# Optimization experiments

Hardware: AMD Instinct MI355X
Metric: run time of the kernel (lower is better)

Reference implementation:

```python
import jax, jax.numpy as jnp
import numpy as np

BN_EPS = 1e-5


def _conv1x1(x, w, b):
    # x: (B, Cin, H, W), w: (Cout, Cin), b: (Cout,)
    return jnp.einsum('bchw,oc->bohw', x, w) + b[None, :, None, None]


def _maxpool2(x):
    b, c, h, w = x.shape
    return x.reshape(b, c, h // 2, 2, w // 2, 2).max(axis=(3, 5))


def setup_inputs() -> dict:
    key = jax.random.key(0)
    ks = jax.random.split(key, 12)
    B, Cc, Cg, H, W = 16, 20, 256, 80, 80
    Ci, Cig = Cc // 2, Cg // 2  # 10, 128
    return {
        'x_c': jax.random.uniform(ks[0], (B, Cc, H, W), jnp.float32),
        'x_1': jax.random.uniform(ks[1], (B, Cg, H, W), jnp.float32),
        'theta_w': jax.random.normal(ks[2], (Ci, Cc), jnp.float32) * 0.1,
        'theta_b': jax.random.normal(ks[3], (Ci,), jnp.float32) * 0.1,
        'phi_w': jax.random.normal(ks[4], (Ci, Cc), jnp.float32) * 0.1,
        'phi_b': jax.random.normal(ks[5], (Ci,), jnp.float32) * 0.1,
        'g_w': jax.random.normal(ks[6], (Cig, Cg), jnp.float32) * 0.05,
        'g_b': jax.random.normal(ks[7], (Cig,), jnp.float32) * 0.05,
        'W_w': jax.random.normal(ks[8], (Cg, Cig), jnp.float32) * 0.05,
        'W_b': jax.random.normal(ks[9], (Cg,), jnp.float32) * 0.05,
        'bn_gamma': jax.random.uniform(ks[10], (Cg,), jnp.float32),
        'bn_beta': jax.random.normal(ks[11], (Cg,), jnp.float32) * 0.1,
    }


def reference(x_c, x_1, theta_w, theta_b, phi_w, phi_b, g_w, g_b, W_w, W_b, bn_gamma, bn_beta):
    B, _, H, W = x_1.shape
    Cig = g_w.shape[0]
    # g path: conv1x1 on x_1 then 2x2 maxpool -> (B, Np, Cig), Np = (H/2)*(W/2)
    g_x = _maxpool2(_conv1x1(x_1, g_w, g_b)).reshape(B, Cig, -1).transpose(0, 2, 1)
    # theta: (B, N, Ci) with N = H*W; phi: (B, Ci, Np)
    theta_x = _conv1x1(x_c, theta_w, theta_b).reshape(B, theta_w.shape[0], -1).transpose(0, 2, 1)
    phi_x = _maxpool2(_conv1x1(x_c, phi_w, phi_b)).reshape(B, phi_w.shape[0], -1)
    f = jnp.einsum('bnc,bcm->bnm', theta_x, phi_x)  # (B, 6400, 1600)
    attn = jax.nn.softmax(f, axis=-1)
    y = jnp.einsum('bnm,bmc->bnc', attn, g_x)  # (B, N, Cig)
    y = y.transpose(0, 2, 1).reshape(B, Cig, H, W)
    # W: conv1x1 + BatchNorm2d (training mode, biased variance)
    w_y = _conv1x1(y, W_w, W_b)
    mean = w_y.mean(axis=(0, 2, 3))
    var = w_y.var(axis=(0, 2, 3))
    w_y = (w_y - mean[None, :, None, None]) * jax.lax.rsqrt(var + BN_EPS)[None, :, None, None]
    w_y = w_y * bn_gamma[None, :, None, None] + bn_beta[None, :, None, None]
    return w_y + x_1
```

## Files before the change

### kernel.cpp

```cpp
#include <hip/hip_runtime.h>
#include <math.h>

#define BB 16
#define CC 20
#define CI 10
#define CG 256
#define CIG 128
#define HH 80
#define WW 80
#define NN 6400
#define HP 40
#define WPD 40
#define NP 1600
#define CNT (BB*NN)

#define OFF_THETA 0
#define OFF_PHI   (OFF_THETA + BB*CI*NN)
#define OFF_Y     (OFF_PHI + BB*CI*NP)
#define OFF_SUMY  (OFF_Y + BB*NN*CIG)
#define OFF_MYY   (OFF_SUMY + 128)
#define OFF_A     (OFF_MYY + 128*128)
#define OFF_BC    (OFF_A + 256)
#define OFF_GW16  (OFF_BC + 256)
#define OFF_WW16  (OFF_GW16 + CG*CIG/2)
#define OFF_GT    (OFF_WW16 + CG*CIG/2)
#define OFF_PARTS (OFF_GT + BB*CIG*NP/2)

typedef _Float16 f16x8 __attribute__((ext_vector_type(8)));
typedef float f32x4 __attribute__((ext_vector_type(4)));
typedef float f32x16 __attribute__((ext_vector_type(16)));

__global__ void k0_prep(const float* __restrict__ gw,
                        const float* __restrict__ ww,
                        float* __restrict__ ws) {
    int idx = blockIdx.x * 256 + threadIdx.x;
    if (idx < CG * CIG) {
        int co = idx / CG, ci = idx % CG;
        _Float16* gw16 = (_Float16*)(ws + OFF_GW16);
        gw16[(ci >> 5) * (CIG * 32) + co * 32 + (ci & 31)] = (_Float16)gw[idx];
        _Float16* ww16 = (_Float16*)(ws + OFF_WW16);
        ww16[idx] = (_Float16)ww[idx];
    }
}

__global__ __launch_bounds__(256) void k1_theta(const float* __restrict__ xc,
                                                const float* __restrict__ tw,
                                                const float* __restrict__ tb,
                                                float* __restrict__ ws) {
    __shared__ float w[CI * CC];
    __shared__ float bia[CI];
    int t = threadIdx.x;
    if (t < CI * CC) w[t] = tw[t];
    if (t < CI) bia[t] = tb[t];
    __syncthreads();
    int idx = blockIdx.x * 256 + t;
    int b = idx / NN, n = idx % NN;
    float acc[CI];
#pragma unroll
    for (int o = 0; o < CI; o++) acc[o] = bia[o];
#pragma unroll
    for (int c = 0; c < CC; c++) {
        float x = xc[(b * CC + c) * NN + n];
#pragma unroll
        for (int o = 0; o < CI; o++) acc[o] += w[o * CC + c] * x;
    }
#pragma unroll
    for (int o = 0; o < CI; o++) ws[OFF_THETA + (b * CI + o) * NN + n] = acc[o];
}

__global__ __launch_bounds__(256) void k1_phi(const float* __restrict__ xc,
                                              const float* __restrict__ pw,
                                              const float* __restrict__ pb,
                                              float* __restrict__ ws) {
    __shared__ float w[CI * CC];
    __shared__ float bia[CI];
    int t = threadIdx.x;
    if (t < CI * CC) w[t] = pw[t];
    if (t < CI) bia[t] = pb[t];
    __syncthreads();
    int idx = blockIdx.x * 256 + t;
    int b = idx / NP, mp = idx % NP;
    int hp = mp / WPD, wp = mp % WPD;
    float best[CI];
#pragma unroll
    for (int o = 0; o < CI; o++) best[o] = -1e30f;
#pragma unroll
    for (int p = 0; p < 4; p++) {
        int n = (2 * hp + (p >> 1)) * WW + 2 * wp + (p & 1);
        float acc[CI];
#pragma unroll
        for (int o = 0; o < CI; o++) acc[o] = bia[o];
#pragma unroll
        for (int c = 0; c < CC; c++) {
            float x = xc[(b * CC + c) * NN + n];
#pragma unroll
            for (int o = 0; o < CI; o++) acc[o] += w[o * CC + c] * x;
        }
#pragma unroll
        for (int o = 0; o < CI; o++) best[o] = fmaxf(best[o], acc[o]);
    }
#pragma unroll
    for (int o = 0; o < CI; o++) ws[OFF_PHI + (b * CI + o) * NP + mp] = best[o];
}

__global__ __launch_bounds__(256) void k2_convg(const float* __restrict__ x1,
                                                const float* __restrict__ gb,
                                                float* __restrict__ ws) {
    __shared__ _Float16 smem[21760];
    const int t = threadIdx.x;
    const int w = t >> 6, l = t & 63, h = l >> 5, ln = l & 31;
    const int bid = blockIdx.x;
    const int b = bid / 40, nb = bid % 40;
    const int n0 = nb * 160;
    const ushort* gw16 = (const ushort*)(ws + OFF_GW16);
    const float* xsrc = x1 + (size_t)b * CG * NN + n0;

    f32x16 acc[5];
#pragma unroll
    for (int j = 0; j < 5; j++)
#pragma unroll
        for (int r = 0; r < 16; r++) acc[j][r] = 0.f;

    const int bk = t >> 3, bs = t & 7;
    uint4 ar[2];
    float4 br[5];

#define K2_LOAD(kc)                                                              \
    {                                                                            \
        ar[0] = *(const uint4*)(gw16 + (kc) * 4096 + t * 16);                    \
        ar[1] = *(const uint4*)(gw16 + (kc) * 4096 + t * 16 + 8);                \
        const float* xr = xsrc + (size_t)((kc) * 32 + bk) * NN + bs * 20;        \
        br[0] = *(const float4*)(xr);                                            \
        br[1] = *(const float4*)(xr + 4);                                        \
        br[2] = *(const float4*)(xr + 8);                                        \
        br[3] = *(const float4*)(xr + 12);                                       \
        br[4] = *(const float4*)(xr + 16);                                       \
    }
#define K2_WRITE(p)                                                              \
    {                                                                            \
        _Float16* Ap = smem + (p) * 10368;                                       \
        _Float16* Bp = Ap + 4608;                                                \
        _Float16* ad = Ap + (t >> 1) * 36 + (t & 1) * 16;                        \
        *(uint2*)(ad + 0) = make_uint2(ar[0].x, ar[0].y);                        \
        *(uint2*)(ad + 4) = make_uint2(ar[0].z, ar[0].w);                        \
        *(uint2*)(ad + 8) = make_uint2(ar[1].x, ar[1].y);                        \
        *(uint2*)(ad + 12) = make_uint2(ar[1].z, ar[1].w);                       \
        _Float16* bd = Bp + bk;                                                  \
        for (int i = 0; i < 5; i++) {                                            \
            int nbase = bs * 20 + 4 * i;                                         \
            bd[(nbase + 0) * 36] = (_Float16)br[i].x;                            \
            bd[(nbase + 1) * 36] = (_Float16)br[i].y;                            \
            bd[(nbase + 2) * 36] = (_Float16)br[i].z;                            \
            bd[(nbase + 3) * 36] = (_Float16)br[i].w;                            \
        }                                                                        \
    }

    K2_LOAD(0);
    K2_WRITE(0);
    __syncthreads();

    for (int kc = 0; kc < 8; ++kc) {
        if (kc < 7) K2_LOAD(kc + 1);
        {
            const _Float16* Ap = smem + (kc & 1) * 10368;
            const _Float16* Bp = Ap + 4608;
#pragma unroll
            for (int kk = 0; kk < 2; kk++) {
                union { f16x8 v; uint2 q[2]; } a;
                const _Float16* ap = Ap + (w * 32 + ln) * 36 + kk * 16 + 8 * h;
                a.q[0] = *(const uint2*)(ap);
                a.q[1] = *(const uint2*)(ap + 4);
#pragma unroll
                for (int j = 0; j < 5; j++) {
                    union { f16x8 v; uint2 q[2]; } bb;
                    const _Float16* bp = Bp + (j * 32 + ln) * 36 + kk * 16 + 8 * h;
                    bb.q[0] = *(const uint2*)(bp);
                    bb.q[1] = *(const uint2*)(bp + 4);
                    acc[j] = __builtin_amdgcn_mfma_f32_32x32x16_f16(a.v, bb.v, acc[j], 0, 0, 0);
                }
            }
        }
        if (kc < 7) {
            K2_WRITE((kc + 1) & 1);
            __syncthreads();
        }
    }

    __syncthreads();
    _Float16* gl = smem;
#pragma unroll
    for (int j = 0; j < 5; j++)
#pragma unroll
        for (int r = 0; r < 16; r++) {
            int co = w * 32 + (r & 3) + 8 * (r >> 2) + 4 * h;
            gl[co * 168 + j * 32 + ln] = (_Float16)acc[j][r];
        }
    __syncthreads();
    {
        int co = t >> 1, qq = t & 1;
        float bias = gb[co];
        union { _Float16 hv[20]; uint2 u[5]; } ov;
        const _Float16* row = gl + co * 168;
#pragma unroll
        for (int o = 0; o < 20; o++) {
            int wp = qq * 20 + o;
            float a0 = (float)row[2 * wp], a1 = (float)row[2 * wp + 1];
            float a2 = (float)row[80 + 2 * wp], a3 = (float)row[81 + 2 * wp];
            ov.hv[o] = (_Float16)(fmaxf(fmaxf(a0, a1), fmaxf(a2, a3)) + bias);
        }
        _Float16* gT = (_Float16*)(ws + OFF_GT) + (size_t)(b * CIG + co) * NP + nb * 40 + qq * 20;
#pragma unroll
        for (int i = 0; i < 5; i++) *(uint2*)(gT + i * 4) = ov.u[i];
    }
#undef K2_LOAD
#undef K2_WRITE
}

__global__ __launch_bounds__(512) void k3_attn(float* __restrict__ ws) {
    __shared__ _Float16 Pt[128][72];
    __shared__ _Float16 gTl[128][72];
    __shared__ float l_run[128];
    __shared__ float psum[2][128];
    __shared__ float sum_l[128];

    const int t = threadIdx.x;
    const int w = t >> 6, l = t & 63;
    const int h = l >> 5, q32 = l & 31;
    const int bid = blockIdx.x;
    const int b = bid / 50, nt = bid % 50, n0 = nt * 128;
    const float* theta = ws + OFF_THETA;
    const float* phi   = ws + OFF_PHI;
    const _Float16* gT = (const _Float16*)(ws + OFF_GT) + (size_t)b * CIG * NP;
    const f32x16 z16 = {0.f,0.f,0.f,0.f,0.f,0.f,0.f,0.f,0.f,0.f,0.f,0.f,0.f,0.f,0.f,0.f};

    const int kt = w & 1;
    const int qt = w >> 1;
    const int ct = w >> 1;
    const int qp0 = 2 * (w & 1), qp1 = qp0 + 1;

    f16x8 thB;
#pragma unroll
    for (int j = 0; j < 8; j++) {
        int c = 8 * h + j;
        thB[j] = (c < CI) ? (_Float16)theta[(b * CI + c) * NN + n0 + qt * 32 + q32]
                          : (_Float16)0.f;
    }

    f32x16 acc0 = z16, acc1 = z16;
    if (t < 128) { l_run[t] = 0.f; sum_l[t] = 0.f; }
    const int cst = t >> 2, gp = t & 3;
    __syncthreads();

    for (int cc = 0; cc < 25; cc++) {
        const int m0 = cc * 64;
        const _Float16* gsrc = gT + (size_t)cst * NP + m0 + gp * 16;
        uint4 ga0 = *(const uint4*)(gsrc);
        uint4 ga1 = *(const uint4*)(gsrc + 8);

        f16x8 phA;
#pragma unroll
        for (int j = 0; j < 8; j++) {
            int c = 8 * h + j;
            phA[j] = (c < CI) ? (_Float16)phi[(b * CI + c) * NP + m0 + kt * 32 + q32]
                              : (_Float16)0.f;
        }
        f32x16 S = __builtin_amdgcn_mfma_f32_32x32x16_f16(phA, thB, z16, 0, 0, 0);

        float ps = 0.f;
#pragma unroll
        for (int G = 0; G < 4; G++) {
            float e0 = __expf(S[4 * G + 0]);
            float e1 = __expf(S[4 * G + 1]);
            float e2 = __expf(S[4 * G + 2]);
            float e3 = __expf(S[4 * G + 3]);
            ps += (e0 + e1) + (e2 + e3);
            union { _Float16 hv[4]; uint2 u; } pk;
            pk.hv[0] = (_Float16)e0; pk.hv[1] = (_Float16)e1;
            pk.hv[2] = (_Float16)e2; pk.hv[3] = (_Float16)e3;
            *(uint2*)&Pt[qt * 32 + q32][kt * 32 + 8 * G + 4 * h] = pk.u;
        }
        ps += __shfl_xor(ps, 32);
        if (l < 32) psum[kt][qt * 32 + l] = ps;

        *(uint4*)&gTl[cst][gp * 16] = ga0;
        *(uint4*)&gTl[cst][gp * 16 + 8] = ga1;
        __syncthreads();

        if (t < 128) l_run[t] += psum[0][t] + psum[1][t];

        __builtin_amdgcn_s_setprio(1);
#pragma unroll
        for (int kk = 0; kk < 4; kk++) {
            f16x8 gA  = *(const f16x8*)&gTl[ct * 32 + q32][kk * 16 + 8 * h];
            f16x8 pB0 = *(const f16x8*)&Pt[qp0 * 32 + q32][kk * 16 + 8 * h];
            f16x8 pB1 = *(const f16x8*)&Pt[qp1 * 32 + q32][kk * 16 + 8 * h];
            acc0 = __builtin_amdgcn_mfma_f32_32x32x16_f16(gA, pB0, acc0, 0, 0, 0);
            acc1 = __builtin_amdgcn_mfma_f32_32x32x16_f16(gA, pB1, acc1, 0, 0, 0);
        }
        __builtin_amdgcn_s_setprio(0);
        __syncthreads();
    }

    const float inv0 = 1.f / l_run[qp0 * 32 + q32];
    const float inv1 = 1.f / l_run[qp1 * 32 + q32];
    float* y = ws + OFF_Y;
    const int nA = n0 + qp0 * 32 + q32;
    const int nB = n0 + qp1 * 32 + q32;
#pragma unroll
    for (int G = 0; G < 4; G++) {
        int c0 = ct * 32 + 8 * G + 4 * h;
        *(float4*)&y[(size_t)(b * NN + nA) * CIG + c0] =
            make_float4(acc0[4 * G + 0] * inv0, acc0[4 * G + 1] * inv0,
                        acc0[4 * G + 2] * inv0, acc0[4 * G + 3] * inv0);
        *(float4*)&y[(size_t)(b * NN + nB) * CIG + c0] =
            make_float4(acc1[4 * G + 0] * inv1, acc1[4 * G + 1] * inv1,
                        acc1[4 * G + 2] * inv1, acc1[4 * G + 3] * inv1);
    }
#pragma unroll
    for (int G = 0; G < 4; G++)
#pragma unroll
        for (int jj = 0; jj < 4; jj++) {
            float v = acc0[4 * G + jj] * inv0 + acc1[4 * G + jj] * inv1;
            v += __shfl_xor(v, 1);
            v += __shfl_xor(v, 2);
            v += __shfl_xor(v, 4);
            v += __shfl_xor(v, 8);
            v += __shfl_xor(v, 16);
            if (q32 == 0) atomicAdd(&sum_l[ct * 32 + 8 * G + 4 * h + jj], v);
        }
    __syncthreads();
    if (t < 128) ws[OFF_PARTS + t * 800 + bid] = sum_l[t];
}

__global__ __launch_bounds__(256) void k3b_reduce(float* __restrict__ ws) {
    __shared__ float red[256];
    const int t = threadIdx.x, co = blockIdx.x;
    const float4* src = (const float4*)(ws + OFF_PARTS + co * 800);
    float s = 0.f;
    for (int i = t; i < 200; i += 256) {
        float4 v = src[i];
        s += (v.x + v.y) + (v.z + v.w);
    }
    red[t] = s;
    __syncthreads();
    for (int off = 128; off > 0; off >>= 1) {
        if (t < off) red[t] += red[t + off];
        __syncthreads();
    }
    if (t == 0) ws[OFF_SUMY + co] = red[0];
}

__global__ __launch_bounds__(512) void k4_stats(float* __restrict__ ws) {
    __shared__ _Float16 ys[64][132];
    __shared__ float ybar_l[128];
    const int t = threadIdx.x;
    const int w = t >> 6, l = t & 63, h = l >> 5, ln = l & 31;
    const int bid = blockIdx.x;
    const float* y = ws + OFF_Y;
    if (t < 128) ybar_l[t] = ws[OFF_SUMY + t] * (1.0f / (float)CNT);
    __syncthreads();

    const int tk = w >> 1;
    const int tl0 = 2 * (w & 1), tl1 = tl0 + 1;

    f32x16 acc0 = {0.f,0.f,0.f,0.f,0.f,0.f,0.f,0.f,0.f,0.f,0.f,0.f,0.f,0.f,0.f,0.f};
    f32x16 acc1 = acc0;

    for (int ch = 0; ch < 10; ch++) {
        const float* ysrc = y + ((size_t)bid * 640 + ch * 64) * CIG;
#pragma unroll
        for (int i = 0; i < 4; i++) {
            int f4 = i * 512 + t;
            int n = f4 >> 5, c4 = (f4 & 31) * 4;
            float4 v = *(const float4*)(ysrc + f4 * 4);
            union { _Float16 hv[4]; uint2 u; } p;
            p.hv[0] = (_Float16)(v.x - ybar_l[c4]);
            p.hv[1] = (_Float16)(v.y - ybar_l[c4 + 1]);
            p.hv[2] = (_Float16)(v.z - ybar_l[c4 + 2]);
            p.hv[3] = (_Float16)(v.w - ybar_l[c4 + 3]);
            *(uint2*)&ys[n][c4] = p.u;
        }
        __syncthreads();
#pragma unroll
        for (int kk = 0; kk < 4; kk++) {
            f16x8 av, bv0, bv1;
#pragma unroll
            for (int j = 0; j < 8; j++) {
                int n = kk * 16 + 8 * h + j;
                av[j]  = ys[n][tk * 32 + ln];
                bv0[j] = ys[n][tl0 * 32 + ln];
                bv1[j] = ys[n][tl1 * 32 + ln];
            }
            acc0 = __builtin_amdgcn_mfma_f32_32x32x16_f16(av, bv0, acc0, 0, 0, 0);
            acc1 = __builtin_amdgcn_mfma_f32_32x32x16_f16(av, bv1, acc1, 0, 0, 0);
        }
        __syncthreads();
    }

    float* Myy = ws + OFF_MYY;
#pragma unroll
    for (int r = 0; r < 16; r++) {
        int k = tk * 32 + (r & 3) + 8 * (r >> 2) + 4 * h;
        atomicAdd(&Myy[k * 128 + tl0 * 32 + ln], acc0[r]);
        atomicAdd(&Myy[k * 128 + tl1 * 32 + ln], acc1[r]);
    }
}

__global__ __launch_bounds__(128) void k5_bnparams(const float* __restrict__ Ww,
                                                   const float* __restrict__ Wb,
                                                   const float* __restrict__ gamma,
                                                   const float* __restrict__ beta,
                                                   float* __restrict__ ws) {
    __shared__ float w[128];
    __shared__ float red[128];
    int t = threadIdx.x;
    int co = blockIdx.x;
    w[t] = Ww[co * CIG + t];
    __syncthreads();
    const float inv_cnt = 1.0f / (float)CNT;

    const float* M = ws + OFF_MYY;
    float tk = 0.f;
#pragma unroll
    for (int l4 = 0; l4 < 32; l4++) {
        float4 m4 = *(const float4*)&M[t * 128 + l4 * 4];
        tk += m4.x * w[l4 * 4] + m4.y * w[l4 * 4 + 1] + m4.z * w[l4 * 4 + 2] + m4.w * w[l4 * 4 + 3];
    }
    red[t] = w[t] * tk;
    __syncthreads();
    for (int off = 64; off > 0; off >>= 1) {
        if (t < off) red[t] += red[t + off];
        __syncthreads();
    }
    if (t == 0) {
        float var = red[0] * inv_cnt;
        float a = gamma[co] * rsqrtf(var + 1e-5f);
        ws[OFF_A + co] = a;
        ws[OFF_BC + co] = beta[co];
    }
}

__global__ __launch_bounds__(256) void k6_final(const float* __restrict__ x1,
                                                float* __restrict__ out,
                                                const float* __restrict__ ws) {
    __shared__ _Float16 k6s[33792];
    __shared__ float ybar_l[128];
    _Float16* Asm = k6s;
    _Float16* Bsm = k6s + 16896;
    const int t = threadIdx.x;
    const int w = t >> 6, l = t & 63, h = l >> 5, ln = l & 31;
    const int bid = blockIdx.x;
    const int b = bid / 100, rr = bid % 100;
    const int nt = rr >> 1, ch = rr & 1;
    const int n0 = nt * 128, co0 = ch * 128;

    if (t < 128) ybar_l[t] = ws[OFF_SUMY + t] * (1.0f / (float)CNT);
    __syncthreads();

    {
        const ushort* wsrc = (const ushort*)(ws + OFF_WW16) + (size_t)co0 * 128;
#pragma unroll
        for (int i = 0; i < 8; i++) {
            int flat = i * 2048 + t * 8;
            uint4 v = *(const uint4*)(wsrc + flat);
            _Float16* dst = Asm + (flat >> 7) * 132 + (flat & 127);
            *(uint2*)(dst) = make_uint2(v.x, v.y);
            *(uint2*)(dst + 4) = make_uint2(v.z, v.w);
        }
    }
    {
        const float* ysrc = ws + OFF_Y + (size_t)(b * NN + n0) * CIG;
#pragma unroll
        for (int i = 0; i < 16; i++) {
            int flat = i * 1024 + t * 4;
            int kcol = flat & 127;
            float4 v = *(const float4*)(ysrc + flat);
            union { _Float16 hv[4]; uint2 u; } p;
            p.hv[0] = (_Float16)(v.x - ybar_l[kcol]);
            p.hv[1] = (_Float16)(v.y - ybar_l[kcol + 1]);
            p.hv[2] = (_Float16)(v.z - ybar_l[kcol + 2]);
            p.hv[3] = (_Float16)(v.w - ybar_l[kcol + 3]);
            *(uint2*)(Bsm + (flat >> 7) * 132 + kcol) = p.u;
        }
    }
    __syncthreads();

    f32x16 acc[4];
#pragma unroll
    for (int j = 0; j < 4; j++)
#pragma unroll
        for (int r = 0; r < 16; r++) acc[j][r] = 0.f;

#pragma unroll
    for (int kk = 0; kk < 8; kk++) {
        union { f16x8 v; uint2 q[2]; } a;
        const _Float16* ap = Asm + (w * 32 + ln) * 132 + kk * 16 + 8 * h;
        a.q[0] = *(const uint2*)(ap);
        a.q[1] = *(const uint2*)(ap + 4);
#pragma unroll
        for (int j = 0; j < 4; j++) {
            union { f16x8 v; uint2 q[2]; } bb;
            const _Float16* bp = Bsm + (j * 32 + ln) * 132 + kk * 16 + 8 * h;
            bb.q[0] = *(const uint2*)(bp);
            bb.q[1] = *(const uint2*)(bp + 4);
            acc[j] = __builtin_amdgcn_mfma_f32_32x32x16_f16(a.v, bb.v, acc[j], 0, 0, 0);
        }
    }

    const float* Av = ws + OFF_A;
    const float* Bc = ws + OFF_BC;
#pragma unroll
    for (int r = 0; r < 16; r++) {
        int cor = co0 + w * 32 + (r & 3) + 8 * (r >> 2) + 4 * h;
        float a = Av[cor], bc = Bc[cor];
        size_t base = (size_t)(b * CG + cor) * NN + n0;
#pragma unroll
        for (int j = 0; j < 4; j++) {
            int n = j * 32 + ln;
            out[base + n] = acc[j][r] * a + bc + x1[base + n];
        }
    }
}

extern "C" void kernel_launch(void* const* d_in, const int* in_sizes, int n_in,
                              void* d_out, int out_size, void* d_ws, size_t ws_size,
                              hipStream_t stream) {
    const float* x_c     = (const float*)d_in[0];
    const float* x_1     = (const float*)d_in[1];
    const float* theta_w = (const float*)d_in[2];
    const float* theta_b = (const float*)d_in[3];
    const float* phi_w   = (const float*)d_in[4];
    const float* phi_b   = (const float*)d_in[5];
    const float* g_w     = (const float*)d_in[6];
    const float* g_b     = (const float*)d_in[7];
    const float* W_w     = (const float*)d_in[8];
    const float* W_b     = (const float*)d_in[9];
    const float* gammap  = (const float*)d_in[10];
    const float* betap   = (const float*)d_in[11];
    float* out = (float*)d_out;
    float* ws  = (float*)d_ws;

    k0_prep<<<128, 256, 0, stream>>>(g_w, W_w, ws);
    k1_theta<<<400, 256, 0, stream>>>(x_c, theta_w, theta_b, ws);
    k1_phi<<<100, 256, 0, stream>>>(x_c, phi_w, phi_b, ws);
    k2_convg<<<640, 256, 0, stream>>>(x_1, g_b, ws);
    hipMemsetAsync(ws + OFF_MYY, 0, (128 * 128) * sizeof(float), stream);
    k3_attn<<<800, 512, 0, stream>>>(ws);
    k3b_reduce<<<128, 256, 0, stream>>>(ws);
    k4_stats<<<160, 512, 0, stream>>>(ws);
    k5_bnparams<<<256, 128, 0, stream>>>(W_w, W_b, gammap, betap, ws);
    k6_final<<<1600, 256, 0, stream>>>(x_1, out, ws);
}
```

Measured before the change: 277.3 us.

## Keep softmax P in registers and double-buffer g tiles in attention kernel

The attention kernel's wave-to-tile mapping changes so each wave owns one 32-query tile across both 32-key halves. This lets the exponentiated scores be rearranged into MFMA B operands with cross-lane shuffles instead of going through a shared-memory P buffer, and the row sums stay in a register. The g tile in shared memory is double-buffered, and the next chunk's g and phi loads are prefetched before the current chunk's MFMAs, leaving one barrier per iteration instead of two. Each wave now computes two score MFMAs per chunk and holds more live registers, which may lower occupancy.

```diff
diff --git a/kernel.cpp b/kernel.cpp
--- a/kernel.cpp
+++ b/kernel.cpp
@@ -217,10 +217,7 @@
 }
 
 __global__ __launch_bounds__(512) void k3_attn(float* __restrict__ ws) {
-    __shared__ _Float16 Pt[128][72];
-    __shared__ _Float16 gTl[128][72];
-    __shared__ float l_run[128];
-    __shared__ float psum[2][128];
+    __shared__ _Float16 gTl[2][128][72];
     __shared__ float sum_l[128];
 
     const int t = threadIdx.x;
@@ -233,10 +230,8 @@
     const _Float16* gT = (const _Float16*)(ws + OFF_GT) + (size_t)b * CIG * NP;
     const f32x16 z16 = {0.f,0.f,0.f,0.f,0.f,0.f,0.f,0.f,0.f,0.f,0.f,0.f,0.f,0.f,0.f,0.f};
 
-    const int kt = w & 1;
-    const int qt = w >> 1;
-    const int ct = w >> 1;
-    const int qp0 = 2 * (w & 1), qp1 = qp0 + 1;
+    const int qt = w & 3, cth = w >> 2;
+    const int ct0 = cth * 2, ct1 = ct0 + 1;
 
     f16x8 thB;
 #pragma unroll
@@ -247,86 +242,132 @@
     }
 
     f32x16 acc0 = z16, acc1 = z16;
-    if (t < 128) { l_run[t] = 0.f; sum_l[t] = 0.f; }
+    float lrun = 0.f;
     const int cst = t >> 2, gp = t & 3;
+    if (t < 128) sum_l[t] = 0.f;
+
+    {
+        const _Float16* gsrc = gT + (size_t)cst * NP + gp * 16;
+        uint4 a0 = *(const uint4*)(gsrc);
+        uint4 a1 = *(const uint4*)(gsrc + 8);
+        *(uint4*)&gTl[0][cst][gp * 16] = a0;
+        *(uint4*)&gTl[0][cst][gp * 16 + 8] = a1;
+    }
+    f16x8 phA0, phA1;
+#pragma unroll
+    for (int j = 0; j < 8; j++) {
+        int c = 8 * h + j;
+        phA0[j] = (c < CI) ? (_Float16)phi[(b * CI + c) * NP + q32] : (_Float16)0.f;
+        phA1[j] = (c < CI) ? (_Float16)phi[(b * CI + c) * NP + 32 + q32] : (_Float16)0.f;
+    }
     __syncthreads();
 
     for (int cc = 0; cc < 25; cc++) {
+        const int cur = cc & 1, nxt = cur ^ 1;
         const int m0 = cc * 64;
-        const _Float16* gsrc = gT + (size_t)cst * NP + m0 + gp * 16;
-        uint4 ga0 = *(const uint4*)(gsrc);
-        uint4 ga1 = *(const uint4*)(gsrc + 8);
-
-        f16x8 phA;
-#pragma unroll
-        for (int j = 0; j < 8; j++) {
-            int c = 8 * h + j;
-            phA[j] = (c < CI) ? (_Float16)phi[(b * CI + c) * NP + m0 + kt * 32 + q32]
-                              : (_Float16)0.f;
-        }
-        f32x16 S = __builtin_amdgcn_mfma_f32_32x32x16_f16(phA, thB, z16, 0, 0, 0);
+
+        f32x16 S0 = __builtin_amdgcn_mfma_f32_32x32x16_f16(phA0, thB, z16, 0, 0, 0);
+        f32x16 S1 = __builtin_amdgcn_mfma_f32_32x32x16_f16(phA1, thB, z16, 0, 0, 0);
+
+        uint4 ga0, ga1;
+        if (cc < 24) {
+            const int m1 = m0 + 64;
+            const _Float16* gsrc = gT + (size_t)cst * NP + m1 + gp * 16;
+            ga0 = *(const uint4*)(gsrc);
+            ga1 = *(const uint4*)(gsrc + 8);
+#pragma unroll
+            for (int j = 0; j < 8; j++) {
+                int c = 8 * h + j;
+                phA0[j] = (c < CI) ? (_Float16)phi[(b * CI + c) * NP + m1 + q32]
+                                   : (_Float16)0.f;
+                phA1[j] = (c < CI) ? (_Float16)phi[(b * CI + c) * NP + m1 + 32 + q32]
+                                   : (_Float16)0.f;
+            }
+        }
 
         float ps = 0.f;
+        uint lo[8], hi[8];
 #pragma unroll
         for (int G = 0; G < 4; G++) {
-            float e0 = __expf(S[4 * G + 0]);
-            float e1 = __expf(S[4 * G + 1]);
-            float e2 = __expf(S[4 * G + 2]);
-            float e3 = __expf(S[4 * G + 3]);
+            float e0 = __expf(S0[4 * G + 0]), e1 = __expf(S0[4 * G + 1]);
+            float e2 = __expf(S0[4 * G + 2]), e3 = __expf(S0[4 * G + 3]);
             ps += (e0 + e1) + (e2 + e3);
-            union { _Float16 hv[4]; uint2 u; } pk;
-            pk.hv[0] = (_Float16)e0; pk.hv[1] = (_Float16)e1;
-            pk.hv[2] = (_Float16)e2; pk.hv[3] = (_Float16)e3;
-            *(uint2*)&Pt[qt * 32 + q32][kt * 32 + 8 * G + 4 * h] = pk.u;
+            union { _Float16 h2[2]; uint u; } pa, pb_;
+            pa.h2[0] = (_Float16)e0; pa.h2[1] = (_Float16)e1;
+            pb_.h2[0] = (_Float16)e2; pb_.h2[1] = (_Float16)e3;
+            lo[G] = pa.u; hi[G] = pb_.u;
+        }
+#pragma unroll
+        for (int G = 0; G < 4; G++) {
+            float e0 = __expf(S1[4 * G + 0]), e1 = __expf(S1[4 * G + 1]);
+            float e2 = __expf(S1[4 * G + 2]), e3 = __expf(S1[4 * G + 3]);
+            ps += (e0 + e1) + (e2 + e3);
+            union { _Float16 h2[2]; uint u; } pa, pb_;
+            pa.h2[0] = (_Float16)e0; pa.h2[1] = (_Float16)e1;
+            pb_.h2[0] = (_Float16)e2; pb_.h2[1] = (_Float16)e3;
+            lo[4 + G] = pa.u; hi[4 + G] = pb_.u;
         }
         ps += __shfl_xor(ps, 32);
-        if (l < 32) psum[kt][qt * 32 + l] = ps;
-
-        *(uint4*)&gTl[cst][gp * 16] = ga0;
-        *(uint4*)&gTl[cst][gp * 16 + 8] = ga1;
+        lrun += ps;
+
+        f16x8 pB[4];
+#pragma unroll
+        for (int kk = 0; kk < 4; kk++) {
+            int i0 = 2 * kk, i1 = 2 * kk + 1;
+            uint pl0 = __shfl_xor(lo[i0], 32), ph0 = __shfl_xor(hi[i0], 32);
+            uint pl1 = __shfl_xor(lo[i1], 32), ph1 = __shfl_xor(hi[i1], 32);
+            union { uint4 u; f16x8 v; } pu;
+            pu.u = (h == 0) ? make_uint4(lo[i0], hi[i0], pl0, ph0)
+                            : make_uint4(pl1, ph1, lo[i1], hi[i1]);
+            pB[kk] = pu.v;
+        }
+
+        __builtin_amdgcn_s_setprio(1);
+#pragma unroll
+        for (int kk = 0; kk < 4; kk++) {
+            f16x8 gA0 = *(const f16x8*)&gTl[cur][ct0 * 32 + q32][kk * 16 + 8 * h];
+            f16x8 gA1 = *(const f16x8*)&gTl[cur][ct1 * 32 + q32][kk * 16 + 8 * h];
+            acc0 = __builtin_amdgcn_mfma_f32_32x32x16_f16(gA0, pB[kk], acc0, 0, 0, 0);
+            acc1 = __builtin_amdgcn_mfma_f32_32x32x16_f16(gA1, pB[kk], acc1, 0, 0, 0);
+        }
+        __builtin_amdgcn_s_setprio(0);
+
+        if (cc < 24) {
+            *(uint4*)&gTl[nxt][cst][gp * 16] = ga0;
+            *(uint4*)&gTl[nxt][cst][gp * 16 + 8] = ga1;
+        }
         __syncthreads();
-
-        if (t < 128) l_run[t] += psum[0][t] + psum[1][t];
-
-        __builtin_amdgcn_s_setprio(1);
-#pragma unroll
-        for (int kk = 0; kk < 4; kk++) {
-            f16x8 gA  = *(const f16x8*)&gTl[ct * 32 + q32][kk * 16 + 8 * h];
-            f16x8 pB0 = *(const f16x8*)&Pt[qp0 * 32 + q32][kk * 16 + 8 * h];
-            f16x8 pB1 = *(const f16x8*)&Pt[qp1 * 32 + q32][kk * 16 + 8 * h];
-            acc0 = __builtin_amdgcn_mfma_f32_32x32x16_f16(gA, pB0, acc0, 0, 0, 0);
-            acc1 = __builtin_amdgcn_mfma_f32_32x32x16_f16(gA, pB1, acc1, 0, 0, 0);
-        }
-        __builtin_amdgcn_s_setprio(0);
-        __syncthreads();
-    }
-
-    const float inv0 = 1.f / l_run[qp0 * 32 + q32];
-    const float inv1 = 1.f / l_run[qp1 * 32 + q32];
+    }
+
+    const float inv = 1.f / lrun;
     float* y = ws + OFF_Y;
-    const int nA = n0 + qp0 * 32 + q32;
-    const int nB = n0 + qp1 * 32 + q32;
+    const int n = n0 + qt * 32 + q32;
 #pragma unroll
     for (int G = 0; G < 4; G++) {
-        int c0 = ct * 32 + 8 * G + 4 * h;
-        *(float4*)&y[(size_t)(b * NN + nA) * CIG + c0] =
-            make_float4(acc0[4 * G + 0] * inv0, acc0[4 * G + 1] * inv0,
-                        acc0[4 * G + 2] * inv0, acc0[4 * G + 3] * inv0);
-        *(float4*)&y[(size_t)(b * NN + nB) * CIG + c0] =
-            make_float4(acc1[4 * G + 0] * inv1, acc1[4 * G + 1] * inv1,
-                        acc1[4 * G + 2] * inv1, acc1[4 * G + 3] * inv1);
+        int c0 = ct0 * 32 + 8 * G + 4 * h;
+        int c1 = ct1 * 32 + 8 * G + 4 * h;
+        *(float4*)&y[(size_t)(b * NN + n) * CIG + c0] =
+            make_float4(acc0[4 * G + 0] * inv, acc0[4 * G + 1] * inv,
+                        acc0[4 * G + 2] * inv, acc0[4 * G + 3] * inv);
+        *(float4*)&y[(size_t)(b * NN + n) * CIG + c1] =
+            make_float4(acc1[4 * G + 0] * inv, acc1[4 * G + 1] * inv,
+                        acc1[4 * G + 2] * inv, acc1[4 * G + 3] * inv);
     }
 #pragma unroll
     for (int G = 0; G < 4; G++)
 #pragma unroll
         for (int jj = 0; jj < 4; jj++) {
-            float v = acc0[4 * G + jj] * inv0 + acc1[4 * G + jj] * inv1;
-            v += __shfl_xor(v, 1);
-            v += __shfl_xor(v, 2);
-            v += __shfl_xor(v, 4);
-            v += __shfl_xor(v, 8);
-            v += __shfl_xor(v, 16);
-            if (q32 == 0) atomicAdd(&sum_l[ct * 32 + 8 * G + 4 * h + jj], v);
+            float v0 = acc0[4 * G + jj] * inv;
+            float v1 = acc1[4 * G + jj] * inv;
+            v0 += __shfl_xor(v0, 1);  v1 += __shfl_xor(v1, 1);
+            v0 += __shfl_xor(v0, 2);  v1 += __shfl_xor(v1, 2);
+            v0 += __shfl_xor(v0, 4);  v1 += __shfl_xor(v1, 4);
+            v0 += __shfl_xor(v0, 8);  v1 += __shfl_xor(v1, 8);
+            v0 += __shfl_xor(v0, 16); v1 += __shfl_xor(v1, 16);
+            if (q32 == 0) {
+                atomicAdd(&sum_l[ct0 * 32 + 8 * G + 4 * h + jj], v0);
+                atomicAdd(&sum_l[ct1 * 32 + 8 * G + 4 * h + jj], v1);
+            }
         }
     __syncthreads();
     if (t < 128) ws[OFF_PARTS + t * 800 + bid] = sum_l[t];
```

Result: slower. 372.3 us (+34.3%).
